# Performance work log

Hardware: AMD Instinct MI355X
Metric: run time of the kernel (lower is better)

## Reference

```python
import jax, jax.numpy as jnp
import numpy as np

D = 1024      # decoder_embed_dim
H = 16        # retention heads
DK = D // H   # q/k head dim = 64
DV = 2 * D // H  # value head dim = 128 (value_embed_dim = 2*embed_dim)
L = 3         # decoder layers
FFN = 4096
S = 1024      # seq len = Lx*Ly
B = 4
V = 2         # vocab
EPS = 1e-6


def layer_norm(x, s, b):
    m = x.mean(-1, keepdims=True)
    v = ((x - m) ** 2).mean(-1, keepdims=True)
    return (x - m) / jnp.sqrt(v + 1e-5) * s + b


def rotate_every_two(x):
    x1 = x[..., ::2]
    x2 = x[..., 1::2]
    return jnp.stack([-x2, x1], axis=-1).reshape(x.shape)


def rel_pos():
    # xpos-style rotary angles + per-head decay mask (torchscale RetNetRelPos)
    angle = 1.0 / (10000.0 ** jnp.linspace(0.0, 1.0, DK // 2))
    angle = jnp.stack([angle, angle], axis=-1).reshape(-1)  # [DK]
    idx = jnp.arange(S)
    sin = jnp.sin(idx[:, None] * angle[None, :])  # [S, DK]
    cos = jnp.cos(idx[:, None] * angle[None, :])
    gamma = 1.0 - 2.0 ** (-5.0 - jnp.arange(H, dtype=jnp.float32))  # [H]
    n = idx[:, None]
    m = idx[None, :]
    expo = jnp.where(n >= m, (n - m).astype(jnp.float32), 0.0)
    dmask = jnp.where(n >= m, gamma[:, None, None] ** expo[None], 0.0)  # [H,S,S]
    dmask = dmask / jnp.sqrt(dmask.sum(-1, keepdims=True))  # row-normalize
    dmask = jnp.nan_to_num(dmask)
    return sin, cos, dmask


def msr(x, Wq, Wk, Wv, Wg, Wo, sin, cos, dmask):
    # multi-scale retention, parallel form
    b, s, _ = x.shape
    q = (x @ Wq).reshape(b, s, H, DK)
    k = (x @ Wk).reshape(b, s, H, DK) * (DK ** -0.5)
    v = (x @ Wv).reshape(b, s, H, DV)
    c = cos[None, :, None, :]
    sn = sin[None, :, None, :]
    q = q * c + rotate_every_two(q) * sn
    k = k * c + rotate_every_two(k) * sn
    qk = jnp.einsum('bnhd,bmhd->bhnm', q, k) * dmask[None]  # [B,H,S,S]
    qk = qk / jnp.clip(jnp.abs(qk).sum(-1, keepdims=True), 1.0, None)
    o = jnp.einsum('bhnm,bmhd->bnhd', qk, v)  # [B,S,H,DV]
    # per-head RMS group norm, no affine
    o = o / jnp.sqrt((o ** 2).mean(-1, keepdims=True) + EPS)
    o = o.reshape(b, s, H * DV)
    o = jax.nn.silu(x @ Wg) * o  # swish gate
    return o @ Wo


def reference(tokens, emb, Wq, Wk, Wv, Wg, Wo, ln1_s, ln1_b, ln2_s, ln2_b,
              W1, b1, W2, b2, lnf_s, lnf_b, Wout):
    shifted = jnp.concatenate(
        [jnp.zeros((tokens.shape[0], 1), tokens.dtype), tokens[:, :-1]], axis=1)
    h = emb[shifted] * jnp.sqrt(jnp.float32(D))
    sin, cos, dmask = rel_pos()
    for l in range(L):
        h = h + msr(layer_norm(h, ln1_s[l], ln1_b[l]),
                    Wq[l], Wk[l], Wv[l], Wg[l], Wo[l], sin, cos, dmask)
        z = layer_norm(h, ln2_s[l], ln2_b[l])
        h = h + (jax.nn.gelu(z @ W1[l] + b1[l]) @ W2[l] + b2[l])
    h = layer_norm(h, lnf_s, lnf_b)
    logits = h @ Wout  # [B,S,V]
    return jax.nn.log_softmax(logits, axis=-1)


def setup_inputs() -> dict:
    key = jax.random.key(0)
    ks = jax.random.split(key, 12)
    sd = 0.02
    return {
        'tokens': jax.random.randint(ks[0], (B, S), 0, V),
        'emb': jax.random.normal(ks[1], (V, D), jnp.float32) * sd,
        'Wq': jax.random.normal(ks[2], (L, D, D), jnp.float32) * sd,
        'Wk': jax.random.normal(ks[3], (L, D, D), jnp.float32) * sd,
        'Wv': jax.random.normal(ks[4], (L, D, 2 * D), jnp.float32) * sd,
        'Wg': jax.random.normal(ks[5], (L, D, 2 * D), jnp.float32) * sd,
        'Wo': jax.random.normal(ks[6], (L, 2 * D, D), jnp.float32) * sd,
        'ln1_s': jnp.ones((L, D), jnp.float32),
        'ln1_b': jnp.zeros((L, D), jnp.float32),
        'ln2_s': jnp.ones((L, D), jnp.float32),
        'ln2_b': jnp.zeros((L, D), jnp.float32),
        'W1': jax.random.normal(ks[7], (L, D, FFN), jnp.float32) * sd,
        'b1': jnp.zeros((L, FFN), jnp.float32),
        'W2': jax.random.normal(ks[8], (L, FFN, D), jnp.float32) * sd,
        'b2': jnp.zeros((L, D), jnp.float32),
        'lnf_s': jnp.ones((D,), jnp.float32),
        'lnf_b': jnp.zeros((D,), jnp.float32),
        'Wout': jax.random.normal(ks[9], (D, V), jnp.float32) * sd,
    }
```

## Files before the change

kernel.cpp:

```cpp
#include <hip/hip_runtime.h>
#include <hip/hip_bf16.h>
#include <math.h>
#include <stdint.h>

#define D_   1024
#define H_   16
#define DK_  64
#define DV_  128
#define L_   3
#define FFN_ 4096
#define S_   1024
#define B_   4
#define NF_  6144

typedef __attribute__((ext_vector_type(8))) _Float16 f16x8;
typedef __attribute__((ext_vector_type(4))) _Float16 f16x4;
typedef __attribute__((ext_vector_type(4))) float f32x4;

__device__ __forceinline__ void gl2lds16(const void* g, void* l) {
    __builtin_amdgcn_global_load_lds(
        (const __attribute__((address_space(1))) void*)(uintptr_t)g,
        (__attribute__((address_space(3))) void*)(uintptr_t)l, 16, 0, 0);
}
#define MFMA16(a,b,c) __builtin_amdgcn_mfma_f32_16x16x32_f16(a,b,c,0,0,0)

__global__ __launch_bounds__(256) void k_embed(const int* __restrict__ tokens,
                                               const float* __restrict__ emb,
                                               float* __restrict__ h) {
    int i = blockIdx.x * 256 + threadIdx.x;
    int d  = i & (D_ - 1);
    int bs = i >> 10;
    int s  = bs & (S_ - 1);
    int b  = bs >> 10;
    int tok = (s == 0) ? 0 : tokens[b * S_ + s - 1];
    h[i] = emb[tok * D_ + d] * 32.0f;
}

__global__ __launch_bounds__(256) void k_ln(const float* __restrict__ x,
                                            const float* __restrict__ s,
                                            const float* __restrict__ b,
                                            _Float16* __restrict__ y) {
    int row = blockIdx.x;
    int t = threadIdx.x;
    const float* xr = x + (size_t)row * D_;
    float4 xv = *(const float4*)&xr[t * 4];
    float sum = xv.x + xv.y + xv.z + xv.w;
    float ssq = xv.x * xv.x + xv.y * xv.y + xv.z * xv.z + xv.w * xv.w;
    __shared__ float sm1[4], sm2[4];
    #pragma unroll
    for (int off = 32; off > 0; off >>= 1) {
        sum += __shfl_down(sum, off, 64);
        ssq += __shfl_down(ssq, off, 64);
    }
    int lane = t & 63, w = t >> 6;
    if (lane == 0) { sm1[w] = sum; sm2[w] = ssq; }
    __syncthreads();
    sum = sm1[0] + sm1[1] + sm1[2] + sm1[3];
    ssq = sm2[0] + sm2[1] + sm2[2] + sm2[3];
    float mean = sum * (1.0f / D_);
    float var  = ssq * (1.0f / D_) - mean * mean;
    float inv  = 1.0f / sqrtf(var + 1e-5f);
    float4 sv = *(const float4*)&s[t * 4];
    float4 bv = *(const float4*)&b[t * 4];
    f16x4 o;
    o.x = (_Float16)((xv.x - mean) * inv * sv.x + bv.x);
    o.y = (_Float16)((xv.y - mean) * inv * sv.y + bv.y);
    o.z = (_Float16)((xv.z - mean) * inv * sv.z + bv.z);
    o.w = (_Float16)((xv.w - mean) * inv * sv.w + bv.w);
    *(f16x4*)&y[(size_t)row * D_ + t * 4] = o;
}

__global__ __launch_bounds__(256) void k_wcast(const float* __restrict__ in,
                                               _Float16* __restrict__ out,
                                               int K, int N) {
    __shared__ float Ts[32][33];
    int n0 = blockIdx.x * 32, k0 = blockIdx.y * 32;
    int t = threadIdx.x;
    #pragma unroll
    for (int c = 0; c < 4; c++) {
        int e = c * 256 + t; int kr = e >> 5, nc = e & 31;
        Ts[kr][nc] = in[(size_t)(k0 + kr) * N + n0 + nc];
    }
    __syncthreads();
    #pragma unroll
    for (int c = 0; c < 4; c++) {
        int e = c * 256 + t; int nr = e >> 5, kc = e & 31;
        out[(size_t)(n0 + nr) * K + k0 + kc] = (_Float16)Ts[kc][nr];
    }
}

__global__ __launch_bounds__(256) void k_gemm_mfma(
    const _Float16* __restrict__ A, const _Float16* __restrict__ Bt,
    const float* __restrict__ bias, float* __restrict__ Cf,
    _Float16* __restrict__ Ch, int M, int N, int K, int flags)
{
    __shared__ __attribute__((aligned(16))) _Float16 As[128 * 32];
    __shared__ __attribute__((aligned(16))) _Float16 Bs[128 * 32];
    int t = threadIdx.x;
    int n0 = blockIdx.x * 128, m0 = blockIdx.y * 128;
    int w = t >> 6, lane = t & 63;
    int quad = lane >> 4, l16 = lane & 15;
    int wm = (w >> 1) * 64, wn = (w & 1) * 64;
    int srow = t >> 1;
    int scg0 = (t & 1) * 2;
    (void)srow; (void)scg0;
    const f16x8* aptr[4]; const f16x8* bptr[4];
    #pragma unroll
    for (int i = 0; i < 4; i++) {
        int ra = wm + i * 16 + l16;
        aptr[i] = (const f16x8*)&As[ra * 32 + ((quad ^ ((ra >> 1) & 3)) * 8)];
        int rb = wn + i * 16 + l16;
        bptr[i] = (const f16x8*)&Bs[rb * 32 + ((quad ^ ((rb >> 1) & 3)) * 8)];
    }
    f32x4 acc[4][4] = {};
    for (int k0 = 0; k0 < K; k0 += 32) {
        __syncthreads();
        #pragma unroll
        for (int c = 0; c < 2; c++) {
            int chunk = c * 256 + t;
            int row = chunk >> 2, cg = chunk & 3;
            int ko = (cg ^ ((row >> 1) & 3)) * 8;
            gl2lds16(A  + (size_t)(m0 + row) * K + k0 + ko, As + chunk * 8);
            gl2lds16(Bt + (size_t)(n0 + row) * K + k0 + ko, Bs + chunk * 8);
        }
        __syncthreads();
        f16x8 af[4], bfr[4];
        #pragma unroll
        for (int i = 0; i < 4; i++) af[i] = *aptr[i];
        #pragma unroll
        for (int j = 0; j < 4; j++) bfr[j] = *bptr[j];
        #pragma unroll
        for (int i = 0; i < 4; i++)
            #pragma unroll
            for (int j = 0; j < 4; j++)
                acc[i][j] = MFMA16(af[i], bfr[j], acc[i][j]);
    }
    #pragma unroll
    for (int i = 0; i < 4; i++) {
        #pragma unroll
        for (int r = 0; r < 4; r++) {
            int row = m0 + wm + i * 16 + quad * 4 + r;
            #pragma unroll
            for (int j = 0; j < 4; j++) {
                int col = n0 + wn + j * 16 + l16;
                float v = acc[i][j][r];
                if (flags & 2) v += bias[col];
                if (flags & 4) v = 0.5f * v * (1.0f + tanhf(0.7978845608f * (v + 0.044715f * v * v * v)));
                if (flags & 8) Ch[(size_t)row * N + col] = (_Float16)v;
                else Cf[(size_t)row * N + col] = v;
            }
        }
    }
}

__global__ __launch_bounds__(256) void k_gemm_splitk(
    const _Float16* __restrict__ A, const _Float16* __restrict__ Bt,
    const float* __restrict__ bias, float* __restrict__ Cf,
    int M, int N, int K, int Kc)
{
    __shared__ __attribute__((aligned(16))) _Float16 As[128 * 32];
    __shared__ __attribute__((aligned(16))) _Float16 Bs[128 * 32];
    int t = threadIdx.x;
    int n0 = blockIdx.x * 128, m0 = blockIdx.y * 128;
    int kc = blockIdx.z;
    const _Float16* Ac  = A  + (size_t)kc * Kc;
    const _Float16* Btc = Bt + (size_t)kc * Kc;
    int w = t >> 6, lane = t & 63;
    int quad = lane >> 4, l16 = lane & 15;
    int wm = (w >> 1) * 64, wn = (w & 1) * 64;
    const f16x8* aptr[4]; const f16x8* bptr[4];
    #pragma unroll
    for (int i = 0; i < 4; i++) {
        int ra = wm + i * 16 + l16;
        aptr[i] = (const f16x8*)&As[ra * 32 + ((quad ^ ((ra >> 1) & 3)) * 8)];
        int rb = wn + i * 16 + l16;
        bptr[i] = (const f16x8*)&Bs[rb * 32 + ((quad ^ ((rb >> 1) & 3)) * 8)];
    }
    f32x4 acc[4][4] = {};
    for (int k0 = 0; k0 < Kc; k0 += 32) {
        __syncthreads();
        #pragma unroll
        for (int c = 0; c < 2; c++) {
            int chunk = c * 256 + t;
            int row = chunk >> 2, cg = chunk & 3;
            int ko = (cg ^ ((row >> 1) & 3)) * 8;
            gl2lds16(Ac  + (size_t)(m0 + row) * K + k0 + ko, As + chunk * 8);
            gl2lds16(Btc + (size_t)(n0 + row) * K + k0 + ko, Bs + chunk * 8);
        }
        __syncthreads();
        f16x8 af[4], bfr[4];
        #pragma unroll
        for (int i = 0; i < 4; i++) af[i] = *aptr[i];
        #pragma unroll
        for (int j = 0; j < 4; j++) bfr[j] = *bptr[j];
        #pragma unroll
        for (int i = 0; i < 4; i++)
            #pragma unroll
            for (int j = 0; j < 4; j++)
                acc[i][j] = MFMA16(af[i], bfr[j], acc[i][j]);
    }
    bool addb = (kc == 0) && (bias != nullptr);
    #pragma unroll
    for (int i = 0; i < 4; i++) {
        #pragma unroll
        for (int r = 0; r < 4; r++) {
            int row = m0 + wm + i * 16 + quad * 4 + r;
            #pragma unroll
            for (int j = 0; j < 4; j++) {
                int col = n0 + wn + j * 16 + l16;
                float v = acc[i][j][r];
                if (addb) v += bias[col];
                atomicAdd(&Cf[(size_t)row * N + col], v);
            }
        }
    }
}

__global__ __launch_bounds__(256) void k_rope(_Float16* __restrict__ x, float scale) {
    int i = blockIdx.x * 256 + threadIdx.x;
    int pair = i & 31;
    int hh = (i >> 5) & 15;
    int bs = i >> 9;
    int sIdx = bs & (S_ - 1);
    float ang = expf(-(float)pair * (1.0f / 31.0f) * 9.210340372f);
    float ph = (float)sIdx * ang;
    float sn, cs;
    sincosf(ph, &sn, &cs);
    size_t base = (size_t)bs * NF_ + hh * DK_ + 2 * pair;
    float x1 = (float)x[base], x2 = (float)x[base + 1];
    x[base]     = (_Float16)((x1 * cs - x2 * sn) * scale);
    x[base + 1] = (_Float16)((x2 * cs + x1 * sn) * scale);
}

__global__ __launch_bounds__(256) void k_vtrans(const _Float16* __restrict__ vb,
                                                _Float16* __restrict__ Vt) {
    int st = blockIdx.x, dt = blockIdx.y, bh = blockIdx.z;
    int hh = bh & 15, b = bh >> 4;
    __shared__ __attribute__((aligned(16))) _Float16 Ts[64][72];
    int t = threadIdx.x;
    const _Float16* src = vb + (size_t)(b * S_ + st * 64) * NF_ + 2048 + hh * DV_ + dt * 64;
    #pragma unroll
    for (int c = 0; c < 2; c++) {
        int chunk = c * 256 + t;
        int r = chunk >> 3, co = (chunk & 7) * 8;
        *(f16x8*)&Ts[r][co] = *(const f16x8*)(src + (size_t)r * NF_ + co);
    }
    __syncthreads();
    _Float16* dst = Vt + ((size_t)bh * DV_ + dt * 64) * S_ + st * 64;
    #pragma unroll
    for (int c = 0; c < 2; c++) {
        int chunk = c * 256 + t;
        int dr = chunk >> 3, so = (chunk & 7) * 8;
        f16x8 val;
        #pragma unroll
        for (int j = 0; j < 8; j++) val[j] = Ts[so + j][dr];
        *(f16x8*)(dst + (size_t)dr * S_ + so) = val;
    }
}

__global__ __launch_bounds__(256) void k_attn(const _Float16* __restrict__ qkvg,
                                              const _Float16* __restrict__ Vt,
                                              float* __restrict__ of) {
    int nt = blockIdx.x, bh = blockIdx.y;
    int hh = bh & 15, b = bh >> 4;
    int t = threadIdx.x, w = t >> 6, lane = t & 63;
    int quad = lane >> 4, l16 = lane & 15;
    int n0 = nt * 64;

    __shared__ __attribute__((aligned(16))) _Float16 Qs[64 * 64];
    __shared__ __attribute__((aligned(16))) _Float16 Ks[64 * 64];
    __shared__ __attribute__((aligned(16))) _Float16 Vs[128 * 64];
    __shared__ __attribute__((aligned(16))) _Float16 Ss[64 * 64];

    const _Float16* qg = qkvg + (size_t)(b * S_ + n0) * NF_ + hh * DK_;
    const _Float16* kg = qkvg + (size_t)(b * S_) * NF_ + 1024 + hh * DK_;
    const _Float16* vg = Vt + (size_t)bh * DV_ * S_;

    #pragma unroll
    for (int c = 0; c < 2; c++) {
        int chunk = c * 256 + t;
        int r = chunk >> 3, cg = chunk & 7;
        int ko = (cg ^ (r & 7)) * 8;
        gl2lds16(qg + (size_t)r * NF_ + ko, Qs + chunk * 8);
    }
    double gd   = 1.0 - exp2((double)(-5 - hh));
    double l2gd = log2(gd);
    float  l2g  = (float)l2gd;
    float rn[4];
    #pragma unroll
    for (int r = 0; r < 4; r++) {
        int n = n0 + w * 16 + quad * 4 + r;
        double rowsum = (1.0 - exp2(l2gd * (double)(n + 1))) / (1.0 - gd);
        rn[r] = (float)(1.0 / sqrt(rowsum));
    }
    int ra = w * 16 + l16;
    const f16x8* qp0 = (const f16x8*)&Qs[ra * 64 + (( quad      ^ (ra & 7)) * 8)];
    const f16x8* qp1 = (const f16x8*)&Qs[ra * 64 + (((quad + 4) ^ (ra & 7)) * 8)];
    const f16x8* sp0 = (const f16x8*)&Ss[ra * 64 + (( quad      ^ (ra & 7)) * 8)];
    const f16x8* sp1 = (const f16x8*)&Ss[ra * 64 + (((quad + 4) ^ (ra & 7)) * 8)];
    const f16x8* kp0[4]; const f16x8* kp1[4];
    const f16x8* vp0[8]; const f16x8* vp1[8];
    #pragma unroll
    for (int j = 0; j < 4; j++) {
        int rb = j * 16 + l16;
        kp0[j] = (const f16x8*)&Ks[rb * 64 + (( quad      ^ (rb & 7)) * 8)];
        kp1[j] = (const f16x8*)&Ks[rb * 64 + (((quad + 4) ^ (rb & 7)) * 8)];
    }
    #pragma unroll
    for (int j = 0; j < 8; j++) {
        int rv = j * 16 + l16;
        vp0[j] = (const f16x8*)&Vs[rv * 64 + (( quad      ^ (rv & 7)) * 8)];
        vp1[j] = (const f16x8*)&Vs[rv * 64 + (((quad + 4) ^ (rv & 7)) * 8)];
    }
    f32x4 oacc[8] = {};
    float absAcc[4] = {};

    for (int mt = 0; mt <= nt; mt++) {
        int m0 = mt * 64;
        __syncthreads();
        #pragma unroll
        for (int c = 0; c < 2; c++) {
            int chunk = c * 256 + t;
            int r = chunk >> 3, cg = chunk & 7;
            int ko = (cg ^ (r & 7)) * 8;
            gl2lds16(kg + (size_t)(m0 + r) * NF_ + ko, Ks + chunk * 8);
        }
        #pragma unroll
        for (int c = 0; c < 4; c++) {
            int chunk = c * 256 + t;
            int r = chunk >> 3, cg = chunk & 7;
            int ko = (cg ^ (r & 7)) * 8;
            gl2lds16(vg + (size_t)r * S_ + m0 + ko, Vs + chunk * 8);
        }
        __syncthreads();
        f16x8 a0 = *qp0, a1 = *qp1;
        f32x4 sacc[4] = {};
        #pragma unroll
        for (int j = 0; j < 4; j++) {
            sacc[j] = MFMA16(a0, *kp0[j], sacc[j]);
            sacc[j] = MFMA16(a1, *kp1[j], sacc[j]);
        }
        #pragma unroll
        for (int j = 0; j < 4; j++) {
            int m = m0 + j * 16 + l16;
            #pragma unroll
            for (int r = 0; r < 4; r++) {
                int n = n0 + w * 16 + quad * 4 + r;
                float dm = (n >= m) ? exp2f((float)(n - m) * l2g) * rn[r] : 0.0f;
                float sv = sacc[j][r] * dm;
                absAcc[r] += fabsf(sv);
                int rowS = w * 16 + quad * 4 + r;
                int colS = j * 16 + l16;
                Ss[rowS * 64 + ((((colS >> 3) ^ (rowS & 7)) << 3) | (colS & 7))] = (_Float16)sv;
            }
        }
        __syncthreads();
        f16x8 s0 = *sp0, s1 = *sp1;
        #pragma unroll
        for (int j = 0; j < 8; j++) {
            oacc[j] = MFMA16(s0, *vp0[j], oacc[j]);
            oacc[j] = MFMA16(s1, *vp1[j], oacc[j]);
        }
    }
    #pragma unroll
    for (int r = 0; r < 4; r++) {
        float s_ = absAcc[r];
        #pragma unroll
        for (int off = 1; off < 16; off <<= 1) s_ += __shfl_xor(s_, off, 64);
        absAcc[r] = s_;
    }
    #pragma unroll
    for (int r = 0; r < 4; r++) {
        int n = n0 + w * 16 + quad * 4 + r;
        float sc = 1.0f / fmaxf(absAcc[r], 1.0f);
        float* og = of + (size_t)(b * S_ + n) * (H_ * DV_) + hh * DV_;
        #pragma unroll
        for (int j = 0; j < 8; j++)
            og[j * 16 + l16] = oacc[j][r] * sc;
    }
}

__global__ __launch_bounds__(256) void k_rmsgate(const float* __restrict__ o,
                                                 const _Float16* __restrict__ qkvg,
                                                 _Float16* __restrict__ out) {
    int row = blockIdx.x * 2 + (threadIdx.x >> 7);
    int tc = threadIdx.x & 127;
    int bs = row >> 4, hh = row & 15;
    size_t obase = (size_t)row * 128 + tc;
    float val = o[obase];
    float gv  = (float)qkvg[(size_t)bs * NF_ + 4096 + hh * DV_ + tc];
    float ss = val * val;
    #pragma unroll
    for (int off = 32; off > 0; off >>= 1) ss += __shfl_down(ss, off, 64);
    __shared__ float sm[4];
    int wv = threadIdx.x >> 6;
    if ((threadIdx.x & 63) == 0) sm[wv] = ss;
    __syncthreads();
    int rw = (threadIdx.x >> 7) * 2;
    ss = sm[rw] + sm[rw + 1];
    float rms = 1.0f / sqrtf(ss * (1.0f / 128.0f) + 1e-6f);
    float sig = 1.0f / (1.0f + expf(-gv));
    out[obase] = (_Float16)(gv * sig * val * rms);
}

__global__ __launch_bounds__(256) void k_final(const float* __restrict__ x,
                                               const float* __restrict__ s,
                                               const float* __restrict__ b,
                                               const float* __restrict__ Wout,
                                               float* __restrict__ out) {
    int row = blockIdx.x;
    int t = threadIdx.x;
    const float* xr = x + (size_t)row * D_;
    float4 xv = *(const float4*)&xr[t * 4];
    float sum = xv.x + xv.y + xv.z + xv.w;
    float ssq = xv.x * xv.x + xv.y * xv.y + xv.z * xv.z + xv.w * xv.w;
    __shared__ float sm1[4], sm2[4];
    #pragma unroll
    for (int off = 32; off > 0; off >>= 1) {
        sum += __shfl_down(sum, off, 64);
        ssq += __shfl_down(ssq, off, 64);
    }
    int lane = t & 63, w = t >> 6;
    if (lane == 0) { sm1[w] = sum; sm2[w] = ssq; }
    __syncthreads();
    sum = sm1[0] + sm1[1] + sm1[2] + sm1[3];
    ssq = sm2[0] + sm2[1] + sm2[2] + sm2[3];
    float mean = sum * (1.0f / D_);
    float var  = ssq * (1.0f / D_) - mean * mean;
    float inv  = 1.0f / sqrtf(var + 1e-5f);
    float4 sv = *(const float4*)&s[t * 4];
    float4 bv = *(const float4*)&b[t * 4];
    float ln[4];
    ln[0] = (xv.x - mean) * inv * sv.x + bv.x;
    ln[1] = (xv.y - mean) * inv * sv.y + bv.y;
    ln[2] = (xv.z - mean) * inv * sv.z + bv.z;
    ln[3] = (xv.w - mean) * inv * sv.w + bv.w;
    float l0 = 0.0f, l1 = 0.0f;
    #pragma unroll
    for (int i = 0; i < 4; i++) {
        int d = t * 4 + i;
        l0 += ln[i] * Wout[d * 2 + 0];
        l1 += ln[i] * Wout[d * 2 + 1];
    }
    #pragma unroll
    for (int off = 32; off > 0; off >>= 1) {
        l0 += __shfl_down(l0, off, 64);
        l1 += __shfl_down(l1, off, 64);
    }
    __syncthreads();
    if (lane == 0) { sm1[w] = l0; sm2[w] = l1; }
    __syncthreads();
    if (t == 0) {
        l0 = sm1[0] + sm1[1] + sm1[2] + sm1[3];
        l1 = sm2[0] + sm2[1] + sm2[2] + sm2[3];
        float mx  = fmaxf(l0, l1);
        float lse = mx + logf(expf(l0 - mx) + expf(l1 - mx));
        out[(size_t)row * 2 + 0] = l0 - lse;
        out[(size_t)row * 2 + 1] = l1 - lse;
    }
}

extern "C" void kernel_launch(void* const* d_in, const int* in_sizes, int n_in,
                              void* d_out, int out_size, void* d_ws, size_t ws_size,
                              hipStream_t stream) {
    const int*   tokens = (const int*)d_in[0];
    const float* emb    = (const float*)d_in[1];
    const float* Wq     = (const float*)d_in[2];
    const float* Wk     = (const float*)d_in[3];
    const float* Wv     = (const float*)d_in[4];
    const float* Wg     = (const float*)d_in[5];
    const float* Wo     = (const float*)d_in[6];
    const float* ln1_s  = (const float*)d_in[7];
    const float* ln1_b  = (const float*)d_in[8];
    const float* ln2_s  = (const float*)d_in[9];
    const float* ln2_b  = (const float*)d_in[10];
    const float* W1     = (const float*)d_in[11];
    const float* b1     = (const float*)d_in[12];
    const float* W2     = (const float*)d_in[13];
    const float* b2     = (const float*)d_in[14];
    const float* lnf_s  = (const float*)d_in[15];
    const float* lnf_b  = (const float*)d_in[16];
    const float* Wout   = (const float*)d_in[17];

    float* ws = (float*)d_ws;
    const size_t M1 = 1u << 20;
    float*     h    = ws;
    _Float16*  x1h  = (_Float16*)(ws + 4 * M1);
    _Float16*  whb  = (_Float16*)(ws + 6 * M1);
    _Float16*  wQKVG= whb;
    _Float16*  woT  = whb + 6 * M1;
    _Float16*  w1T  = whb + 8 * M1;
    _Float16*  w2T  = whb + 12 * M1;
    _Float16*  qkvg = (_Float16*)(ws + 14 * M1);
    _Float16*  Vth  = (_Float16*)(ws + 27 * M1);
    float*     of   = ws + 31 * M1;
    _Float16*  oh   = (_Float16*)(ws + 27 * M1);
    _Float16*  f1h  = (_Float16*)(ws + 14 * M1);

    k_embed<<<16384, 256, 0, stream>>>(tokens, emb, h);

    for (int l = 0; l < L_; l++) {
        const float* pWq = Wq + (size_t)l * M1;
        const float* pWk = Wk + (size_t)l * M1;
        const float* pWv = Wv + (size_t)l * 2 * M1;
        const float* pWg = Wg + (size_t)l * 2 * M1;
        const float* pWo = Wo + (size_t)l * 2 * M1;
        const float* pW1 = W1 + (size_t)l * 4 * M1;
        const float* pW2 = W2 + (size_t)l * 4 * M1;

        k_wcast<<<dim3(32, 32),  256, 0, stream>>>(pWq, wQKVG,          1024, 1024);
        k_wcast<<<dim3(32, 32),  256, 0, stream>>>(pWk, wQKVG + 1 * M1, 1024, 1024);
        k_wcast<<<dim3(64, 32),  256, 0, stream>>>(pWv, wQKVG + 2 * M1, 1024, 2048);
        k_wcast<<<dim3(64, 32),  256, 0, stream>>>(pWg, wQKVG + 4 * M1, 1024, 2048);
        k_wcast<<<dim3(32, 64),  256, 0, stream>>>(pWo, woT, 2048, 1024);
        k_wcast<<<dim3(128, 32), 256, 0, stream>>>(pW1, w1T, 1024, 4096);
        k_wcast<<<dim3(32, 128), 256, 0, stream>>>(pW2, w2T, 4096, 1024);

        k_ln<<<4096, 256, 0, stream>>>(h, ln1_s + l * D_, ln1_b + l * D_, x1h);
        k_gemm_mfma<<<dim3(48, 32), 256, 0, stream>>>(x1h, wQKVG, nullptr, nullptr, qkvg,
                                                      4096, NF_, 1024, 8);
        k_rope<<<8192, 256, 0, stream>>>(qkvg, 1.0f);
        k_rope<<<8192, 256, 0, stream>>>(qkvg + 1024, 0.125f);
        k_vtrans<<<dim3(16, 2, 64), 256, 0, stream>>>(qkvg, Vth);
        k_attn<<<dim3(16, 64), 256, 0, stream>>>(qkvg, Vth, of);
        k_rmsgate<<<32768, 256, 0, stream>>>(of, qkvg, oh);
        k_gemm_splitk<<<dim3(8, 32, 2), 256, 0, stream>>>(oh, woT, nullptr, h,
                                                          4096, 1024, 2048, 1024);
        k_ln<<<4096, 256, 0, stream>>>(h, ln2_s + l * D_, ln2_b + l * D_, x1h);
        k_gemm_mfma<<<dim3(32, 32), 256, 0, stream>>>(x1h, w1T, b1 + l * FFN_, nullptr, f1h,
                                                      4096, 4096, 1024, 2 | 4 | 8);
        k_gemm_splitk<<<dim3(8, 32, 4), 256, 0, stream>>>(f1h, w2T, b2 + l * D_, h,
                                                          4096, 1024, 4096, 1024);
    }
    k_final<<<4096, 256, 0, stream>>>(h, lnf_s, lnf_b, Wout, (float*)d_out);
}
```

Baseline: 1.584 ms.

## Replace split-K atomics with partial buffers reduced in layernorm, add tile swizzle

Split-K GEMMs now write their partial sums to two separate fp32 buffers instead of doing atomicAdd into the residual. The following layernorm, or the final kernel, adds both partials to the residual and writes it back. GEMM grids also become 1D, and a grouped tile swizzle walks 8x8 tile groups to improve L2 reuse. The FFN down-projection now uses 2 K-chunks instead of 4, trading fewer blocks for no atomics but extra partial-buffer traffic.

```diff
diff --git a/kernel.cpp b/kernel.cpp
--- a/kernel.cpp
+++ b/kernel.cpp
@@ -23,6 +23,15 @@
         (__attribute__((address_space(3))) void*)(uintptr_t)l, 16, 0, 0);
 }
 #define MFMA16(a,b,c) __builtin_amdgcn_mfma_f32_16x16x32_f16(a,b,c,0,0,0)
+
+__device__ __forceinline__ void tile_swizzle(int pid, int N, int* m0, int* n0) {
+    int nb = N >> 7;
+    int sgn = nb >> 3;
+    int sid = pid >> 6, wi = pid & 63;
+    int smi = sid / sgn, sni = sid - smi * sgn;
+    *m0 = ((smi << 3) + (wi >> 3)) << 7;
+    *n0 = ((sni << 3) + (wi & 7)) << 7;
+}
 
 __global__ __launch_bounds__(256) void k_embed(const int* __restrict__ tokens,
                                                const float* __restrict__ emb,
@@ -36,14 +45,24 @@
     h[i] = emb[tok * D_ + d] * 32.0f;
 }
 
-__global__ __launch_bounds__(256) void k_ln(const float* __restrict__ x,
+__global__ __launch_bounds__(256) void k_ln(float* __restrict__ x,
+                                            const float* __restrict__ p0,
+                                            const float* __restrict__ p1,
+                                            int np,
                                             const float* __restrict__ s,
                                             const float* __restrict__ b,
                                             _Float16* __restrict__ y) {
     int row = blockIdx.x;
     int t = threadIdx.x;
-    const float* xr = x + (size_t)row * D_;
-    float4 xv = *(const float4*)&xr[t * 4];
+    size_t base = (size_t)row * D_ + t * 4;
+    float4 xv = *(float4*)&x[base];
+    if (np) {
+        float4 a = *(const float4*)&p0[base];
+        float4 c = *(const float4*)&p1[base];
+        xv.x += a.x + c.x; xv.y += a.y + c.y;
+        xv.z += a.z + c.z; xv.w += a.w + c.w;
+        *(float4*)&x[base] = xv;
+    }
     float sum = xv.x + xv.y + xv.z + xv.w;
     float ssq = xv.x * xv.x + xv.y * xv.y + xv.z * xv.z + xv.w * xv.w;
     __shared__ float sm1[4], sm2[4];
@@ -67,7 +86,7 @@
     o.y = (_Float16)((xv.y - mean) * inv * sv.y + bv.y);
     o.z = (_Float16)((xv.z - mean) * inv * sv.z + bv.z);
     o.w = (_Float16)((xv.w - mean) * inv * sv.w + bv.w);
-    *(f16x4*)&y[(size_t)row * D_ + t * 4] = o;
+    *(f16x4*)&y[base] = o;
 }
 
 __global__ __launch_bounds__(256) void k_wcast(const float* __restrict__ in,
@@ -97,13 +116,11 @@
     __shared__ __attribute__((aligned(16))) _Float16 As[128 * 32];
     __shared__ __attribute__((aligned(16))) _Float16 Bs[128 * 32];
     int t = threadIdx.x;
-    int n0 = blockIdx.x * 128, m0 = blockIdx.y * 128;
+    int m0, n0;
+    tile_swizzle(blockIdx.x, N, &m0, &n0);
     int w = t >> 6, lane = t & 63;
     int quad = lane >> 4, l16 = lane & 15;
     int wm = (w >> 1) * 64, wn = (w & 1) * 64;
-    int srow = t >> 1;
-    int scg0 = (t & 1) * 2;
-    (void)srow; (void)scg0;
     const f16x8* aptr[4]; const f16x8* bptr[4];
     #pragma unroll
     for (int i = 0; i < 4; i++) {
@@ -155,16 +172,18 @@
 
 __global__ __launch_bounds__(256) void k_gemm_splitk(
     const _Float16* __restrict__ A, const _Float16* __restrict__ Bt,
-    const float* __restrict__ bias, float* __restrict__ Cf,
+    const float* __restrict__ bias, float* __restrict__ P,
     int M, int N, int K, int Kc)
 {
     __shared__ __attribute__((aligned(16))) _Float16 As[128 * 32];
     __shared__ __attribute__((aligned(16))) _Float16 Bs[128 * 32];
     int t = threadIdx.x;
-    int n0 = blockIdx.x * 128, m0 = blockIdx.y * 128;
+    int m0, n0;
+    tile_swizzle(blockIdx.x, N, &m0, &n0);
     int kc = blockIdx.z;
     const _Float16* Ac  = A  + (size_t)kc * Kc;
     const _Float16* Btc = Bt + (size_t)kc * Kc;
+    float* Pz = P + (size_t)kc * M * N;
     int w = t >> 6, lane = t & 63;
     int quad = lane >> 4, l16 = lane & 15;
     int wm = (w >> 1) * 64, wn = (w & 1) * 64;
@@ -210,7 +229,7 @@
                 int col = n0 + wn + j * 16 + l16;
                 float v = acc[i][j][r];
                 if (addb) v += bias[col];
-                atomicAdd(&Cf[(size_t)row * N + col], v);
+                Pz[(size_t)row * N + col] = v;
             }
         }
     }
@@ -404,14 +423,22 @@
 }
 
 __global__ __launch_bounds__(256) void k_final(const float* __restrict__ x,
+                                               const float* __restrict__ p0,
+                                               const float* __restrict__ p1,
                                                const float* __restrict__ s,
                                                const float* __restrict__ b,
                                                const float* __restrict__ Wout,
                                                float* __restrict__ out) {
     int row = blockIdx.x;
     int t = threadIdx.x;
-    const float* xr = x + (size_t)row * D_;
-    float4 xv = *(const float4*)&xr[t * 4];
+    size_t base = (size_t)row * D_ + t * 4;
+    float4 xv = *(const float4*)&x[base];
+    {
+        float4 a = *(const float4*)&p0[base];
+        float4 c = *(const float4*)&p1[base];
+        xv.x += a.x + c.x; xv.y += a.y + c.y;
+        xv.z += a.z + c.z; xv.w += a.w + c.w;
+    }
     float sum = xv.x + xv.y + xv.z + xv.w;
     float ssq = xv.x * xv.x + xv.y * xv.y + xv.z * xv.z + xv.w * xv.w;
     __shared__ float sm1[4], sm2[4];
@@ -496,6 +523,8 @@
     float*     of   = ws + 31 * M1;
     _Float16*  oh   = (_Float16*)(ws + 27 * M1);
     _Float16*  f1h  = (_Float16*)(ws + 14 * M1);
+    float*     pb0  = ws + 31 * M1;
+    float*     pb1  = ws + 35 * M1;
 
     k_embed<<<16384, 256, 0, stream>>>(tokens, emb, h);
 
@@ -516,21 +545,23 @@
         k_wcast<<<dim3(128, 32), 256, 0, stream>>>(pW1, w1T, 1024, 4096);
         k_wcast<<<dim3(32, 128), 256, 0, stream>>>(pW2, w2T, 4096, 1024);
 
-        k_ln<<<4096, 256, 0, stream>>>(h, ln1_s + l * D_, ln1_b + l * D_, x1h);
-        k_gemm_mfma<<<dim3(48, 32), 256, 0, stream>>>(x1h, wQKVG, nullptr, nullptr, qkvg,
-                                                      4096, NF_, 1024, 8);
+        k_ln<<<4096, 256, 0, stream>>>(h, pb0, pb1, (l == 0) ? 0 : 1,
+                                       ln1_s + l * D_, ln1_b + l * D_, x1h);
+        k_gemm_mfma<<<dim3(1536), 256, 0, stream>>>(x1h, wQKVG, nullptr, nullptr, qkvg,
+                                                    4096, NF_, 1024, 8);
         k_rope<<<8192, 256, 0, stream>>>(qkvg, 1.0f);
         k_rope<<<8192, 256, 0, stream>>>(qkvg + 1024, 0.125f);
         k_vtrans<<<dim3(16, 2, 64), 256, 0, stream>>>(qkvg, Vth);
         k_attn<<<dim3(16, 64), 256, 0, stream>>>(qkvg, Vth, of);
         k_rmsgate<<<32768, 256, 0, stream>>>(of, qkvg, oh);
-        k_gemm_splitk<<<dim3(8, 32, 2), 256, 0, stream>>>(oh, woT, nullptr, h,
-                                                          4096, 1024, 2048, 1024);
-        k_ln<<<4096, 256, 0, stream>>>(h, ln2_s + l * D_, ln2_b + l * D_, x1h);
-        k_gemm_mfma<<<dim3(32, 32), 256, 0, stream>>>(x1h, w1T, b1 + l * FFN_, nullptr, f1h,
-                                                      4096, 4096, 1024, 2 | 4 | 8);
-        k_gemm_splitk<<<dim3(8, 32, 4), 256, 0, stream>>>(f1h, w2T, b2 + l * D_, h,
-                                                          4096, 1024, 4096, 1024);
-    }
-    k_final<<<4096, 256, 0, stream>>>(h, lnf_s, lnf_b, Wout, (float*)d_out);
-}
+        k_gemm_splitk<<<dim3(256, 1, 2), 256, 0, stream>>>(oh, woT, nullptr, pb0,
+                                                           4096, 1024, 2048, 1024);
+        k_ln<<<4096, 256, 0, stream>>>(h, pb0, pb1, 1,
+                                       ln2_s + l * D_, ln2_b + l * D_, x1h);
+        k_gemm_mfma<<<dim3(1024), 256, 0, stream>>>(x1h, w1T, b1 + l * FFN_, nullptr, f1h,
+                                                    4096, 4096, 1024, 2 | 4 | 8);
+        k_gemm_splitk<<<dim3(256, 1, 2), 256, 0, stream>>>(f1h, w2T, b2 + l * D_, pb0,
+                                                           4096, 1024, 4096, 2048);
+    }
+    k_final<<<4096, 256, 0, stream>>>(h, pb0, pb1, lnf_s, lnf_b, Wout, (float*)d_out);
+}
```

After: 1.478 ms. 6.7% less time.
